# Kernel tuning notes

Measured on AMD Instinct MI355X. Metric: run time of the kernel, lower is better.

Reference implementation:

```python
import jax, jax.numpy as jnp
import numpy as np
from jax import lax

# init_kwargs constants
DO_TUBE = False
TAU = 0.3
ITERATIONS = 5
BLEND_FACTOR = 0.3


def _avg_pool3(x):
    """3x3x3 avg pool, stride 1, zero padding 1, count_include_pad=True.
    x: (n, h, w, d). Matches torch F.avg_pool3d(kernel=3, stride=1, padding=1)."""
    s = lax.reduce_window(x, 0.0, lax.add, (1, 3, 3, 3), (1, 1, 1, 1), 'SAME')
    return s * (1.0 / 27.0)


def setup_inputs() -> dict:
    key = jax.random.key(0)
    # binary mask (b, 1, h, w, d) as docstring requires
    u = jax.random.uniform(key, (2, 1, 256, 256, 256), dtype=jnp.float32)
    seg = (u > 0.5).astype(jnp.float32)
    return {"segmentation": seg}


def reference(segmentation):
    b, c, h, w, d = segmentation.shape
    x = segmentation.reshape(b * c, h, w, d)

    # NOTE: in the original code `mask` is never updated inside the iteration
    # loop, so every iteration adds the identical term; the loop over the
    # batch dim is also trivially batchable. Compute the per-iteration term
    # once (fully batched) and scale by ITERATIONS.
    eroded = -_avg_pool3(-x)            # differentiable erosion
    dilated = _avg_pool3(eroded)        # differentiable dilation
    diff = x - dilated
    term = jax.nn.sigmoid((diff - 0.5) / TAU) + diff  # soft_threshold + residual
    skeleton = ITERATIONS * term

    skeleton = skeleton.reshape(b, c, h, w, d)
    # DO_TUBE is False (the torch code path for True is broken for 5D input)
    skeleton = BLEND_FACTOR * segmentation + (1.0 - BLEND_FACTOR) * skeleton
    skeleton = jnp.round(jnp.clip(skeleton, 0.0, 1.0))
    return 1.0 - skeleton
```

## Files before the change

### kernel.cpp

```cpp
#include <hip/hip_runtime.h>
#include <stdint.h>


typedef float        vfloat4 __attribute__((ext_vector_type(4)));
typedef unsigned int vuint4  __attribute__((ext_vector_type(4)));

#define CH2 32
#define BLOCKS 1024

__global__ __launch_bounds__(256) void skel_fused(const float* __restrict__ x,
                                                  float* __restrict__ outp) {
    __shared__ vfloat4 lds[2][8][64];
    const int ln  = threadIdx.x & 63;
    const int wv  = threadIdx.x >> 6;
    const int bid = blockIdx.x;
    const int L      = (bid & 7) * 128 + (bid >> 3);
    const int wblock = L >> 4;
    const int combo  = L & 15;
    const int b      = combo & 1;
    const int hc     = combo >> 1;
    const int w0b    = wblock * 4;
    const int w      = w0b + wv;
    const int h0     = hc * CH2;

    const vfloat4* __restrict__ xs = (const vfloat4*)x;
    vfloat4* __restrict__ os = (vfloat4*)outp;
    const uint32_t rbase = (uint32_t)b * 4194304u + (uint32_t)w * 64u + (uint32_t)ln;
    const vfloat4 vzero = {0.0f, 0.0f, 0.0f, 0.0f};

    const int sr0 = w0b - 2 + 2 * wv, sr1 = sr0 + 1;
    const int sc0 = sr0 < 0 ? 0 : (sr0 > 255 ? 255 : sr0);
    const int sc1 = sr1 < 0 ? 0 : (sr1 > 255 ? 255 : sr1);
    const uint32_t sb0 = (uint32_t)b * 4194304u + (uint32_t)sc0 * 64u + (uint32_t)ln;
    const uint32_t sb1 = (uint32_t)b * 4194304u + (uint32_t)sc1 * 64u + (uint32_t)ln;

    auto stage = [&](int hp, int buf) {
        int hcl = hp < 0 ? 0 : (hp > 255 ? 255 : hp);
        uint32_t off = (uint32_t)hcl * 16384u;
        __builtin_amdgcn_global_load_lds(
            (const __attribute__((address_space(1))) void*)&xs[sb0 + off],
            (__attribute__((address_space(3))) void*)&lds[buf][2 * wv][0],
            16, 0, 0);
        __builtin_amdgcn_global_load_lds(
            (const __attribute__((address_space(1))) void*)&xs[sb1 + off],
            (__attribute__((address_space(3))) void*)&lds[buf][2 * wv + 1][0],
            16, 0, 0);
    };

    bool cv[5];
    #pragma unroll
    for (int j = 0; j < 5; ++j) {
        int wj = w + j - 2;
        cv[j] = (wj >= 0) && (wj <= 255);
    }

    auto dw_from = [&](int buf, int hp) -> uint32_t {
        if (hp < 0 || hp > 255) return 0u;
        vfloat4 R[5];
        #pragma unroll
        for (int j = 0; j < 5; ++j) {
            vfloat4 v = lds[buf][wv + j][ln];
            R[j] = cv[j] ? v : vzero;
        }
        vfloat4 s = R[0] + R[4] + 2.0f * (R[1] + R[3]) + 3.0f * R[2];
        if (w == 0 || w == 255) s = s - R[2];
        uint32_t tn = (uint32_t)s.x | ((uint32_t)s.y << 8)
                    | ((uint32_t)s.z << 16) | ((uint32_t)s.w << 24);
        vuint4 u2 = __builtin_bit_cast(vuint4, R[2]);
        uint32_t tx = ((u2.x >> 22) & 0x80u)    | ((u2.y >> 14) & 0x8000u)
                    | ((u2.z >> 6) & 0x800000u) | ((u2.w << 2) & 0x80000000u);
        uint32_t up = (uint32_t)__shfl_up((int)tn, 1);
        uint32_t dn = (uint32_t)__shfl_down((int)tn, 1);
        if (ln == 0)  up = 0u;
        if (ln == 63) dn = 0u;
        uint64_t W = (uint64_t)(up >> 16) | ((uint64_t)tn << 16)
                   | ((uint64_t)(dn & 0xffffu) << 48);
        uint64_t S = W + ((W >> 8) << 1) + (W >> 16) * 3u + ((W >> 24) << 1) + (W >> 32);
        uint32_t n = (uint32_t)S;
        if (ln == 0)  n -= (tn & 0xffu);
        if (ln == 63) n -= (tn & 0xff000000u);
        return n | tx;
    };

    auto emit = [&](int h, uint32_t a0, uint32_t a1, uint32_t a2,
                    uint32_t a3, uint32_t a4) {
        uint32_t m0 = a0 & 0x7f7f7f7fu, m1 = a1 & 0x7f7f7f7fu, m2 = a2 & 0x7f7f7f7fu,
                 m3 = a3 & 0x7f7f7f7fu, m4 = a4 & 0x7f7f7f7fu;
        uint32_t e0 = m0 & 0x00ff00ffu, e1 = m1 & 0x00ff00ffu, e2 = m2 & 0x00ff00ffu,
                 e3 = m3 & 0x00ff00ffu, e4 = m4 & 0x00ff00ffu;
        uint32_t o0 = (m0 >> 8) & 0x00ff00ffu, o1 = (m1 >> 8) & 0x00ff00ffu,
                 o2 = (m2 >> 8) & 0x00ff00ffu, o3 = (m3 >> 8) & 0x00ff00ffu,
                 o4 = (m4 >> 8) & 0x00ff00ffu;
        uint32_t ae = e0 + e4 + ((e1 + e3) << 1) + e2 * 3u;
        uint32_t ao = o0 + o4 + ((o1 + o3) << 1) + o2 * 3u;
        if (h == 0 || h == 255) { ae -= e2; ao -= o2; }
        vfloat4 o;
        o.x = (((ae & 0xffffu) >= 9u) && !(a2 & 0x80u))       ? 1.0f : 0.0f;
        o.y = (((ao & 0xffffu) >= 9u) && !(a2 & 0x8000u))     ? 1.0f : 0.0f;
        o.z = (((ae >> 16) >= 9u)     && !(a2 & 0x800000u))   ? 1.0f : 0.0f;
        o.w = (((ao >> 16) >= 9u)     && !(a2 & 0x80000000u)) ? 1.0f : 0.0f;
        __builtin_nontemporal_store(o, &os[rbase + (uint32_t)h * 16384u]);
    };

    stage(h0 - 2, 0);
    __syncthreads();
    stage(h0 - 1, 1);
    uint32_t d0 = 0, d1 = 0, d2 = 0, d3 = 0;
    int cur = 0;
    const int plast = h0 + CH2 + 1;
    for (int p = h0 - 2; p <= plast; ++p) {
        uint32_t d4 = dw_from(cur, p);
        if (p >= h0 + 2) emit(p - 2, d0, d1, d2, d3, d4);
        __syncthreads();
        if (p + 2 <= plast) stage(p + 2, cur);
        cur ^= 1;
        d0 = d1; d1 = d2; d2 = d3; d3 = d4;
    }
}

extern "C" void kernel_launch(void* const* d_in, const int* in_sizes, int n_in,
                              void* d_out, int out_size, void* d_ws, size_t ws_size,
                              hipStream_t stream) {
    const float* x = (const float*)d_in[0];
    skel_fused<<<BLOCKS, 256, 0, stream>>>(x, (float*)d_out);
}
```

Baseline: 240.0 us.

## Process two h-planes per barrier with a four-slot LDS ring buffer

The LDS staging buffer grows from two slots to four, indexed by plane modulo four. Each loop iteration now handles two h-planes, so there is one barrier per two planes instead of one per plane. Prefetches for the next two planes are issued before the current planes are computed, and the emits are reordered to run before the compute. The aim is to halve synchronization overhead and give loads more time in flight, at the cost of doubled LDS use per block and a larger register window.

```diff
diff --git a/kernel.cpp b/kernel.cpp
--- a/kernel.cpp
+++ b/kernel.cpp
@@ -10,7 +10,7 @@
 
 __global__ __launch_bounds__(256) void skel_fused(const float* __restrict__ x,
                                                   float* __restrict__ outp) {
-    __shared__ vfloat4 lds[2][8][64];
+    __shared__ vfloat4 lds[4][8][64];
     const int ln  = threadIdx.x & 63;
     const int wv  = threadIdx.x >> 6;
     const int bid = blockIdx.x;
@@ -34,7 +34,8 @@
     const uint32_t sb0 = (uint32_t)b * 4194304u + (uint32_t)sc0 * 64u + (uint32_t)ln;
     const uint32_t sb1 = (uint32_t)b * 4194304u + (uint32_t)sc1 * 64u + (uint32_t)ln;
 
-    auto stage = [&](int hp, int buf) {
+    auto stage = [&](int hp) {
+        int buf = (hp + 8) & 3;
         int hcl = hp < 0 ? 0 : (hp > 255 ? 255 : hp);
         uint32_t off = (uint32_t)hcl * 16384u;
         __builtin_amdgcn_global_load_lds(
@@ -54,8 +55,9 @@
         cv[j] = (wj >= 0) && (wj <= 255);
     }
 
-    auto dw_from = [&](int buf, int hp) -> uint32_t {
+    auto dw_from = [&](int hp) -> uint32_t {
         if (hp < 0 || hp > 255) return 0u;
+        int buf = (hp + 8) & 3;
         vfloat4 R[5];
         #pragma unroll
         for (int j = 0; j < 5; ++j) {
@@ -102,20 +104,23 @@
         __builtin_nontemporal_store(o, &os[rbase + (uint32_t)h * 16384u]);
     };
 
-    stage(h0 - 2, 0);
-    __syncthreads();
-    stage(h0 - 1, 1);
-    uint32_t d0 = 0, d1 = 0, d2 = 0, d3 = 0;
-    int cur = 0;
     const int plast = h0 + CH2 + 1;
-    for (int p = h0 - 2; p <= plast; ++p) {
-        uint32_t d4 = dw_from(cur, p);
-        if (p >= h0 + 2) emit(p - 2, d0, d1, d2, d3, d4);
+    stage(h0 - 2); stage(h0 - 1);
+    uint32_t Wd[8] = {0, 0, 0, 0, 0, 0, 0, 0};
+    for (int p = h0 - 2; p <= plast; p += 2) {
         __syncthreads();
-        if (p + 2 <= plast) stage(p + 2, cur);
-        cur ^= 1;
-        d0 = d1; d1 = d2; d2 = d3; d3 = d4;
+        if (p + 2 <= plast) { stage(p + 2); stage(p + 3); }
+        if (p >= h0 + 4) {
+            emit(p - 4, Wd[2], Wd[3], Wd[4], Wd[5], Wd[6]);
+            emit(p - 3, Wd[3], Wd[4], Wd[5], Wd[6], Wd[7]);
+        }
+        uint32_t da = dw_from(p);
+        uint32_t db = dw_from(p + 1);
+        Wd[0] = Wd[2]; Wd[1] = Wd[3]; Wd[2] = Wd[4]; Wd[3] = Wd[5];
+        Wd[4] = Wd[6]; Wd[5] = Wd[7]; Wd[6] = da; Wd[7] = db;
     }
+    emit(plast - 3, Wd[2], Wd[3], Wd[4], Wd[5], Wd[6]);
+    emit(plast - 2, Wd[3], Wd[4], Wd[5], Wd[6], Wd[7]);
 }
 
 extern "C" void kernel_launch(void* const* d_in, const int* in_sizes, int n_in,
```

New measurement: 250.8 us. 1.04x slower.
